# Performance work log

Hardware: AMD Instinct MI355X
Metric: run time of the kernel (lower is better)

Reference implementation:

```python
import jax, jax.numpy as jnp
import numpy as np

N_BINS = 15


def setup_inputs() -> dict:
    key = jax.random.key(0)
    k1, k2 = jax.random.split(key)
    N, C = 65536, 1000
    logits = jax.random.normal(k1, (N, C), dtype=jnp.float32)
    labels = jax.random.randint(k2, (N,), 0, C, dtype=jnp.int64)
    return {"logits": logits, "labels": labels}


def reference(logits, labels):
    # softmax confidences, per-class correctness indicators
    N, C = logits.shape
    conf = jax.nn.softmax(logits, axis=1)                       # [N, C]
    acc = (jnp.arange(C)[None, :] == labels[:, None]).astype(conf.dtype)  # [N, C]

    # Bin assignment replicating (conf > lower) & (conf <= upper) with
    # boundaries linspace(0,1,n_bins+1): bin b covers (b/n_bins, (b+1)/n_bins].
    # conf == 0 falls in no bin -> route to dummy segment N_BINS.
    bin_idx = jnp.clip(jnp.ceil(conf * N_BINS).astype(jnp.int32) - 1, 0, N_BINS - 1)
    bin_idx = jnp.where(conf > 0.0, bin_idx, N_BINS)            # [N, C]
    col_idx = jnp.broadcast_to(jnp.arange(C, dtype=jnp.int32), (N, C))

    # Fused per-(bin, class) histogram scatter: counts, sum conf, sum acc.
    zeros = jnp.zeros((N_BINS + 1, C), dtype=conf.dtype)
    counts = zeros.at[bin_idx, col_idx].add(1.0)[:N_BINS]        # [B, C]
    sum_conf = zeros.at[bin_idx, col_idx].add(conf)[:N_BINS]     # [B, C]
    sum_acc = zeros.at[bin_idx, col_idx].add(acc)[:N_BINS]       # [B, C]

    prob_in_bin = counts / N
    safe = jnp.maximum(counts, 1.0)
    avg_conf = sum_conf / safe
    avg_acc = sum_acc / safe
    per_bin = jnp.where(counts > 0, jnp.abs(avg_conf - avg_acc) * prob_in_bin, 0.0)
    ece = jnp.sum(per_bin) / C
    return ece.reshape(1)
```

## Files before the change

kernel.cpp:

```cpp
#include <hip/hip_runtime.h>
#include <math.h>

#define NBINS   15
#define CDIM    1000
#define QDIM    250
#define HIST_ELEMS (NBINS * CDIM)
#define THREADS 512
#define NWAVES  (THREADS / 64)
#define PAD     -1000.0f

__device__ __forceinline__ float waveSum(float v) {
#pragma unroll
    for (int o = 32; o > 0; o >>= 1) v += __shfl_xor(v, o, 64);
    return v;
}

__device__ __forceinline__ void loadRow(float4 (&v)[4], int& label,
                                        const float* __restrict__ logits,
                                        const int* __restrict__ labels,
                                        int r, int lane) {
    const float4* row = (const float4*)(logits + (size_t)r * CDIM);
#pragma unroll
    for (int j = 0; j < 4; ++j) {
        int q = lane + 64 * j;
        v[j] = (q < QDIM) ? row[q] : make_float4(PAD, PAD, PAD, PAD);
    }
    label = labels[r];
}

__device__ __forceinline__ void computeRow(float4 (&v)[4], int label, int lane,
                                           float (&regAcc)[4][4],
                                           float* __restrict__ sB,
                                           float* __restrict__ D) {
    float s = 0.0f, m = 0.0f;
#pragma unroll
    for (int j = 0; j < 4; ++j) {
        v[j].x = __expf(v[j].x);
        v[j].y = __expf(v[j].y);
        v[j].z = __expf(v[j].z);
        v[j].w = __expf(v[j].w);
        s += (v[j].x + v[j].y) + (v[j].z + v[j].w);
        m = fmaxf(m, fmaxf(fmaxf(v[j].x, v[j].y), fmaxf(v[j].z, v[j].w)));
    }
    s = waveSum(s);
    const float inv = 1.0f / s;

    const float cmax = m * inv;
    const bool  rare = __any(cmax * 15.0f > 1.0f);

    if (!rare) {
#pragma unroll
        for (int j = 0; j < 4; ++j) {
            regAcc[j][0] = fmaf(v[j].x, inv, regAcc[j][0]);
            regAcc[j][1] = fmaf(v[j].y, inv, regAcc[j][1]);
            regAcc[j][2] = fmaf(v[j].z, inv, regAcc[j][2]);
            regAcc[j][3] = fmaf(v[j].w, inv, regAcc[j][3]);
        }
        const int lq = label >> 2;
        const int lk = label & 3;
        if (lane == (lq & 63))
            unsafeAtomicAdd(&sB[lk * QDIM + lq], -1.0f);
    } else {
#pragma unroll
        for (int j = 0; j < 4; ++j) {
            const int q = lane + 64 * j;
            const float cf[4] = {v[j].x, v[j].y, v[j].z, v[j].w};
#pragma unroll
            for (int k = 0; k < 4; ++k) {
                float conf = cf[k] * inv;
                float t    = conf * 15.0f;
                float add  = conf - ((4 * q + k == label) ? 1.0f : 0.0f);
                if (t > 1.0f) {
                    int b = min((int)ceilf(t) - 1, NBINS - 1);
                    unsafeAtomicAdd(&D[b * CDIM + k * QDIM + q], add);
                } else {
                    regAcc[j][k] += add;
                }
            }
        }
    }
}

__global__ __launch_bounds__(THREADS, 4) void ece_hist_kernel(
        const float* __restrict__ logits,
        const int*   __restrict__ labels,
        float*       __restrict__ D,
        int N, int rowsPerBlock)
{
    __shared__ float sB[CDIM];

    const int tid  = threadIdx.x;
    const int lane = tid & 63;
    const int w    = tid >> 6;

    for (int i = tid; i < CDIM; i += THREADS) sB[i] = 0.0f;
    __syncthreads();

    const int r0 = blockIdx.x * rowsPerBlock;
    const int r1 = min(r0 + rowsPerBlock, N);

    float regAcc[4][4];
#pragma unroll
    for (int j = 0; j < 4; ++j)
#pragma unroll
        for (int k = 0; k < 4; ++k) regAcc[j][k] = 0.0f;

    float4 vA[4], vB[4], vC[4];
    int    lA = 0, lB = 0, lC = 0;

    int rA = r0 + w;
    int rB = rA + NWAVES;
    int rC = rB + NWAVES;

    if (rA < r1) loadRow(vA, lA, logits, labels, rA, lane);
    if (rB < r1) loadRow(vB, lB, logits, labels, rB, lane);
    if (rC < r1) loadRow(vC, lC, logits, labels, rC, lane);

    while (rA < r1) {
        computeRow(vA, lA, lane, regAcc, sB, D);
        rA = rC + NWAVES;
        if (rA < r1) loadRow(vA, lA, logits, labels, rA, lane);

        if (rB >= r1) break;
        computeRow(vB, lB, lane, regAcc, sB, D);
        rB = rA + NWAVES;
        if (rB < r1) loadRow(vB, lB, logits, labels, rB, lane);

        if (rC >= r1) break;
        computeRow(vC, lC, lane, regAcc, sB, D);
        rC = rB + NWAVES;
        if (rC < r1) loadRow(vC, lC, logits, labels, rC, lane);
    }

#pragma unroll
    for (int j = 0; j < 4; ++j) {
        int q = lane + 64 * j;
        if (q < QDIM) {
#pragma unroll
            for (int k = 0; k < 4; ++k)
                unsafeAtomicAdd(&sB[k * QDIM + q], regAcc[j][k]);
        }
    }

    __syncthreads();
    for (int i = tid; i < CDIM; i += THREADS) {
        float val = sB[i];
        if (val != 0.0f) unsafeAtomicAdd(&D[i], val);
    }
}

__global__ __launch_bounds__(1024) void ece_final_kernel(
        const float* __restrict__ D, float* __restrict__ out, float scale)
{
    float s = 0.0f;
    const float4* D4 = (const float4*)D;
    for (int i = threadIdx.x; i < HIST_ELEMS / 4; i += 1024) {
        float4 t = D4[i];
        s += (fabsf(t.x) + fabsf(t.y)) + (fabsf(t.z) + fabsf(t.w));
    }
    s = waveSum(s);
    __shared__ float sr[16];
    const int lane = threadIdx.x & 63;
    const int wid  = threadIdx.x >> 6;
    if (lane == 0) sr[wid] = s;
    __syncthreads();
    if (threadIdx.x == 0) {
        float t = 0.0f;
#pragma unroll
        for (int ww = 0; ww < 16; ++ww) t += sr[ww];
        out[0] = t * scale;
    }
}

extern "C" void kernel_launch(void* const* d_in, const int* in_sizes, int n_in,
                              void* d_out, int out_size, void* d_ws, size_t ws_size,
                              hipStream_t stream)
{
    const float* logits = (const float*)d_in[0];
    const int*   labels = (const int*)d_in[1];

    const int N = in_sizes[1];

    float* D = (float*)d_ws;
    hipMemsetAsync(D, 0, HIST_ELEMS * sizeof(float), stream);

    const int grid = 512;
    const int rowsPerBlock = (N + grid - 1) / grid;

    ece_hist_kernel<<<grid, THREADS, 0, stream>>>(logits, labels, D, N, rowsPerBlock);

    const float scale = 1.0f / ((float)N * (float)CDIM);
    ece_final_kernel<<<1, 1024, 0, stream>>>(D, (float*)d_out, scale);
}
```

Before: 71.05 us.

## Replace triple-buffered row prefetch with simple loop and raise occupancy

Removes the three-row register software pipeline and processes one row per iteration with an unrolled-off loop, freeing registers. Block size drops to 256 threads with min 5 blocks per CU and the grid grows to 1280 blocks, so latency is hidden by more resident waves rather than explicit prefetch. The risk is that with fewer in-flight loads per wave, memory-level parallelism depends entirely on occupancy, and more blocks mean more per-block flushes of the shared histogram to global atomics.

Measured after the change: 85.56 us. 1.2x slower.

```diff
diff --git a/kernel.cpp b/kernel.cpp
--- a/kernel.cpp
+++ b/kernel.cpp
@@ -5,7 +5,7 @@
 #define CDIM    1000
 #define QDIM    250
 #define HIST_ELEMS (NBINS * CDIM)
-#define THREADS 512
+#define THREADS 256
 #define NWAVES  (THREADS / 64)
 #define PAD     -1000.0f
 
@@ -13,19 +13,6 @@
 #pragma unroll
     for (int o = 32; o > 0; o >>= 1) v += __shfl_xor(v, o, 64);
     return v;
-}
-
-__device__ __forceinline__ void loadRow(float4 (&v)[4], int& label,
-                                        const float* __restrict__ logits,
-                                        const int* __restrict__ labels,
-                                        int r, int lane) {
-    const float4* row = (const float4*)(logits + (size_t)r * CDIM);
-#pragma unroll
-    for (int j = 0; j < 4; ++j) {
-        int q = lane + 64 * j;
-        v[j] = (q < QDIM) ? row[q] : make_float4(PAD, PAD, PAD, PAD);
-    }
-    label = labels[r];
 }
 
 __device__ __forceinline__ void computeRow(float4 (&v)[4], int label, int lane,
@@ -81,7 +68,7 @@
     }
 }
 
-__global__ __launch_bounds__(THREADS, 4) void ece_hist_kernel(
+__global__ __launch_bounds__(THREADS, 5) void ece_hist_kernel(
         const float* __restrict__ logits,
         const int*   __restrict__ labels,
         float*       __restrict__ D,
@@ -105,31 +92,18 @@
 #pragma unroll
         for (int k = 0; k < 4; ++k) regAcc[j][k] = 0.0f;
 
-    float4 vA[4], vB[4], vC[4];
-    int    lA = 0, lB = 0, lC = 0;
+#pragma clang loop unroll(disable)
+    for (int r = r0 + w; r < r1; r += NWAVES) {
+        float4 v[4];
+        const float4* row = (const float4*)(logits + (size_t)r * CDIM);
+        v[0] = row[lane];
+        v[1] = row[lane + 64];
+        v[2] = row[lane + 128];
+        v[3] = (lane < QDIM - 192) ? row[lane + 192]
+                                   : make_float4(PAD, PAD, PAD, PAD);
+        const int label = labels[r];
 
-    int rA = r0 + w;
-    int rB = rA + NWAVES;
-    int rC = rB + NWAVES;
-
-    if (rA < r1) loadRow(vA, lA, logits, labels, rA, lane);
-    if (rB < r1) loadRow(vB, lB, logits, labels, rB, lane);
-    if (rC < r1) loadRow(vC, lC, logits, labels, rC, lane);
-
-    while (rA < r1) {
-        computeRow(vA, lA, lane, regAcc, sB, D);
-        rA = rC + NWAVES;
-        if (rA < r1) loadRow(vA, lA, logits, labels, rA, lane);
-
-        if (rB >= r1) break;
-        computeRow(vB, lB, lane, regAcc, sB, D);
-        rB = rA + NWAVES;
-        if (rB < r1) loadRow(vB, lB, logits, labels, rB, lane);
-
-        if (rC >= r1) break;
-        computeRow(vC, lC, lane, regAcc, sB, D);
-        rC = rB + NWAVES;
-        if (rC < r1) loadRow(vC, lC, logits, labels, rC, lane);
+        computeRow(v, label, lane, regAcc, sB, D);
     }
 
 #pragma unroll
@@ -184,7 +158,7 @@
     float* D = (float*)d_ws;
     hipMemsetAsync(D, 0, HIST_ELEMS * sizeof(float), stream);
 
-    const int grid = 512;
+    const int grid = 1280;
     const int rowsPerBlock = (N + grid - 1) / grid;
 
     ece_hist_kernel<<<grid, THREADS, 0, stream>>>(logits, labels, D, N, rowsPerBlock);
```
